# Optimization experiments

Measured on AMD Instinct MI355X. Metric: run time of the kernel, lower is better.

## Reference

```python
import jax, jax.numpy as jnp
import numpy as np

B, S, D = 4, 2048, 512   # batch, seq_len, head_size (== d_model)
H = 8                    # num_heads
DH = D // H              # depth per head = 64


def setup_inputs() -> dict:
    key = jax.random.key(0)
    ks = jax.random.split(key, 11)
    sc = 1.0 / np.sqrt(D)
    inp = {
        "q": jax.random.normal(ks[0], (B, S, D), jnp.float32),
        "k": jax.random.normal(ks[1], (B, S, D), jnp.float32),
        "v": jax.random.normal(ks[2], (B, S, D), jnp.float32),
        # causal mask: 1.0 where attention is disallowed (j > i)
        "mask": jnp.triu(jnp.ones((S, S), jnp.float32), k=1)[None, None, :, :],
        "wq": jax.random.normal(ks[3], (D, D), jnp.float32) * sc,
        "bq": jnp.zeros((D,), jnp.float32),
        "wk": jax.random.normal(ks[4], (D, D), jnp.float32) * sc,
        "bk": jnp.zeros((D,), jnp.float32),
        "wv": jax.random.normal(ks[5], (D, D), jnp.float32) * sc,
        "bv": jnp.zeros((D,), jnp.float32),
        "wo": jax.random.normal(ks[6], (D, D), jnp.float32) * sc,
        "bo": jnp.zeros((D,), jnp.float32),
    }
    return inp


def _split_heads(x):
    # [B,S,D] -> [B,H,S,DH]
    return x.reshape(B, S, H, DH).transpose(0, 2, 1, 3)


def reference(q, k, v, mask, wq, bq, wk, bk, wv, bv, wo, bo):
    query = _split_heads(q @ wq + bq)
    key_h = _split_heads(k @ wk + bk)
    value = _split_heads(v @ wv + bv)

    scale = 1.0 / jnp.sqrt(jnp.asarray(DH, jnp.float32))
    scores = jnp.einsum("bhqd,bhkd->bhqk", query, key_h) * scale
    scores = scores + mask * -1e9
    attn = jax.nn.softmax(scores, axis=-1)  # [B,H,S,S]

    ctx = jnp.einsum("bhqk,bhkd->bhqd", attn, value)
    ctx = ctx.transpose(0, 2, 1, 3).reshape(B, S, D)  # concat heads
    out = ctx @ wo + bo
    return out, attn
```

## Files before the change

kernel.cpp:

```cpp
#include <hip/hip_runtime.h>

#define Bq 4
#define Sq 2048
#define Dq 512
#define Hq 8
#define DHq 64

typedef __attribute__((ext_vector_type(8))) short bf16x8;
typedef __attribute__((ext_vector_type(4))) float floatx4;

__device__ __forceinline__ unsigned short f2bf(float f) {
    union { float f; unsigned u; } v; v.f = f;
    return (unsigned short)((v.u + 0x7fffu + ((v.u >> 16) & 1u)) >> 16);
}

template <bool OUT_BF16>
__global__ __launch_bounds__(256) void gemm_bias(
    const float* A0, const float* A1, const float* A2,
    const float* W0, const float* W1, const float* W2,
    const float* b0, const float* b1, const float* b2,
    unsigned short* O0, unsigned short* O1, unsigned short* O2,
    float* F0, float* F1, float* F2) {
  const int bz = blockIdx.z;
  const float* A = (bz == 0) ? A0 : (bz == 1) ? A1 : A2;
  const float* W = (bz == 0) ? W0 : (bz == 1) ? W1 : W2;
  const float* bias = (bz == 0) ? b0 : (bz == 1) ? b1 : b2;
  unsigned short* O = (bz == 0) ? O0 : (bz == 1) ? O1 : O2;
  float* F = (bz == 0) ? F0 : (bz == 1) ? F1 : F2;

  const int bm = blockIdx.x;
  const int bn = blockIdx.y;
  const int tid = threadIdx.x;
  const int lane = tid & 63;
  const int w = tid >> 6;
  const int wm = w >> 1;
  const int wn = w & 1;
  const int lg = lane >> 4;
  const int lc = lane & 15;

  __shared__ unsigned short As[4096];
  __shared__ unsigned short Bs[4096];

  floatx4 acc[4][4];
#pragma unroll
  for (int mt = 0; mt < 4; ++mt)
#pragma unroll
    for (int nt = 0; nt < 4; ++nt) acc[mt][nt] = (floatx4){0.f, 0.f, 0.f, 0.f};

  for (int kt = 0; kt < 16; ++kt) {
    __syncthreads();
#pragma unroll
    for (int it = 0; it < 4; ++it) {
      int idx = tid + it * 256;
      int m = idx >> 3;
      int k0 = (idx & 7) << 2;
      const float4 va =
          *(const float4*)(A + (size_t)(bm * 128 + m) * 512 + kt * 32 + k0);
      union { unsigned short u[4]; uint2 v; } pk;
      pk.u[0] = f2bf(va.x); pk.u[1] = f2bf(va.y);
      pk.u[2] = f2bf(va.z); pk.u[3] = f2bf(va.w);
      *(uint2*)&As[((((k0 >> 3) * 128 + m)) << 3) + (k0 & 7)] = pk.v;
    }
#pragma unroll
    for (int it = 0; it < 4; ++it) {
      int e = tid + it * 256;
      int n = e & 127;
      int k0 = (e >> 7) << 2;
      union { unsigned short u[4]; uint2 v; } pk;
#pragma unroll
      for (int u = 0; u < 4; ++u)
        pk.u[u] = f2bf(W[(size_t)(kt * 32 + k0 + u) * 512 + bn * 128 + n]);
      *(uint2*)&Bs[((((k0 >> 3) * 128 + n)) << 3) + (k0 & 7)] = pk.v;
    }
    __syncthreads();

    bf16x8 af[4], bfr[4];
#pragma unroll
    for (int mt = 0; mt < 4; ++mt)
      af[mt] = *(const bf16x8*)&As[(lg * 128 + wm * 64 + mt * 16 + lc) << 3];
#pragma unroll
    for (int nt = 0; nt < 4; ++nt)
      bfr[nt] = *(const bf16x8*)&Bs[(lg * 128 + wn * 64 + nt * 16 + lc) << 3];
#pragma unroll
    for (int mt = 0; mt < 4; ++mt)
#pragma unroll
      for (int nt = 0; nt < 4; ++nt)
        acc[mt][nt] = __builtin_amdgcn_mfma_f32_16x16x32_bf16(
            af[mt], bfr[nt], acc[mt][nt], 0, 0, 0);
  }

#pragma unroll
  for (int mt = 0; mt < 4; ++mt) {
#pragma unroll
    for (int nt = 0; nt < 4; ++nt) {
      int col = bn * 128 + wn * 64 + nt * 16 + lc;
      float bv = bias[col];
#pragma unroll
      for (int r = 0; r < 4; ++r) {
        int row = bm * 128 + wm * 64 + mt * 16 + lg * 4 + r;
        float val = acc[mt][nt][r] + bv;
        if (OUT_BF16)
          O[(size_t)row * 512 + col] = f2bf(val);
        else
          F[(size_t)row * 512 + col] = val;
      }
    }
  }
}

__global__ __launch_bounds__(256) void attn_kernel(
    const unsigned short* Qb, const unsigned short* Kb,
    const unsigned short* Vb, float* attn, float* ctx) {
  const int qt = blockIdx.x;
  const int h = blockIdx.y;
  const int b = blockIdx.z;
  const int qb = qt * 64;
  const int tid = threadIdx.x;
  const int lane = tid & 63;
  const int w = tid >> 6;
  const int lg = lane >> 4;
  const int lc = lane & 15;

  __shared__ unsigned short Qs[4096], Ks[4096], Vs[4096], Ps[4096];

#pragma unroll
  for (int it = 0; it < 2; ++it) {
    int cc = tid + it * 256;
    int koct = cc & 7, m = cc >> 3;
    *(uint4*)&Qs[((koct << 6) + m) << 3] =
        *(const uint4*)&Qb[(size_t)(b * Sq + qb + m) * Dq + h * DHq +
                           (koct << 3)];
  }
  __syncthreads();

  bf16x8 aQ[2];
#pragma unroll
  for (int ks = 0; ks < 2; ++ks)
    aQ[ks] = *(const bf16x8*)&Qs[(((ks * 4 + lg) << 6) + (w * 16 + lc)) << 3];

  float mrun[4] = {-1e30f, -1e30f, -1e30f, -1e30f};
  float lrun[4] = {0.f, 0.f, 0.f, 0.f};
  const int qi_base = qb + w * 16 + lg * 4;

  for (int jt = 0; jt <= qt; ++jt) {
    __syncthreads();
#pragma unroll
    for (int it = 0; it < 2; ++it) {
      int cc = tid + it * 256;
      int koct = cc & 7, m = cc >> 3;
      *(uint4*)&Ks[((koct << 6) + m) << 3] =
          *(const uint4*)&Kb[(size_t)(b * Sq + jt * 64 + m) * Dq + h * DHq +
                             (koct << 3)];
    }
    __syncthreads();

    floatx4 s[4];
#pragma unroll
    for (int nt = 0; nt < 4; ++nt) s[nt] = (floatx4){0.f, 0.f, 0.f, 0.f};
#pragma unroll
    for (int ks = 0; ks < 2; ++ks)
#pragma unroll
      for (int nt = 0; nt < 4; ++nt) {
        bf16x8 bk =
            *(const bf16x8*)&Ks[(((ks * 4 + lg) << 6) + nt * 16 + lc) << 3];
        s[nt] = __builtin_amdgcn_mfma_f32_16x16x32_bf16(aQ[ks], bk, s[nt], 0,
                                                        0, 0);
      }

#pragma unroll
    for (int r = 0; r < 4; ++r) {
      int qi = qi_base + r;
      float sv[4];
      float mx = -1e30f;
#pragma unroll
      for (int nt = 0; nt < 4; ++nt) {
        float x = s[nt][r] * 0.125f;
        int kj = jt * 64 + nt * 16 + lc;
        if (kj > qi) x = -1e30f;
        sv[nt] = x;
        mx = fmaxf(mx, x);
      }
#pragma unroll
      for (int off = 1; off < 16; off <<= 1)
        mx = fmaxf(mx, __shfl_xor(mx, off, 16));
      float mnew = fmaxf(mrun[r], mx);
      float sum = 0.f;
#pragma unroll
      for (int nt = 0; nt < 4; ++nt) sum += __expf(sv[nt] - mnew);
#pragma unroll
      for (int off = 1; off < 16; off <<= 1) sum += __shfl_xor(sum, off, 16);
      lrun[r] = lrun[r] * __expf(mrun[r] - mnew) + sum;
      mrun[r] = mnew;
    }
  }

  float rinv[4];
#pragma unroll
  for (int r = 0; r < 4; ++r) rinv[r] = 1.0f / lrun[r];

  floatx4 ctxa[4];
#pragma unroll
  for (int nt = 0; nt < 4; ++nt) ctxa[nt] = (floatx4){0.f, 0.f, 0.f, 0.f};

  float* attn_base = attn + (size_t)(b * Hq + h) * Sq * Sq;

  for (int jt = 0; jt <= qt; ++jt) {
    __syncthreads();
#pragma unroll
    for (int it = 0; it < 2; ++it) {
      int cc = tid + it * 256;
      int koct = cc & 7, m = cc >> 3;
      *(uint4*)&Ks[((koct << 6) + m) << 3] =
          *(const uint4*)&Kb[(size_t)(b * Sq + jt * 64 + m) * Dq + h * DHq +
                             (koct << 3)];
    }
#pragma unroll
    for (int it = 0; it < 2; ++it) {
      int cc = tid + it * 256;
      int dim = cc & 63, koct = cc >> 6;
      union { unsigned short u[8]; uint4 v; } pk;
#pragma unroll
      for (int u = 0; u < 8; ++u)
        pk.u[u] = Vb[(size_t)(b * Sq + jt * 64 + koct * 8 + u) * Dq + h * DHq +
                     dim];
      *(uint4*)&Vs[((koct << 6) + dim) << 3] = pk.v;
    }
    __syncthreads();

    floatx4 s[4];
#pragma unroll
    for (int nt = 0; nt < 4; ++nt) s[nt] = (floatx4){0.f, 0.f, 0.f, 0.f};
#pragma unroll
    for (int ks = 0; ks < 2; ++ks)
#pragma unroll
      for (int nt = 0; nt < 4; ++nt) {
        bf16x8 bk =
            *(const bf16x8*)&Ks[(((ks * 4 + lg) << 6) + nt * 16 + lc) << 3];
        s[nt] = __builtin_amdgcn_mfma_f32_16x16x32_bf16(aQ[ks], bk, s[nt], 0,
                                                        0, 0);
      }

#pragma unroll
    for (int r = 0; r < 4; ++r) {
      int qi = qi_base + r;
      float* arow = attn_base + (size_t)qi * Sq + jt * 64;
#pragma unroll
      for (int nt = 0; nt < 4; ++nt) {
        int kj = jt * 64 + nt * 16 + lc;
        float x = s[nt][r] * 0.125f;
        float p = (kj > qi) ? 0.f : __expf(x - mrun[r]) * rinv[r];
        arow[nt * 16 + lc] = p;
        int kk = nt * 16 + lc;
        Ps[w * 1024 + (((kk >> 3) * 16 + lg * 4 + r) << 3) + (kk & 7)] =
            f2bf(p);
      }
    }

#pragma unroll
    for (int ks = 0; ks < 2; ++ks) {
      bf16x8 ap =
          *(const bf16x8*)&Ps[w * 1024 + (((ks * 4 + lg) * 16 + lc) << 3)];
#pragma unroll
      for (int nt = 0; nt < 4; ++nt) {
        bf16x8 bv =
            *(const bf16x8*)&Vs[(((ks * 4 + lg) << 6) + nt * 16 + lc) << 3];
        ctxa[nt] = __builtin_amdgcn_mfma_f32_16x16x32_bf16(ap, bv, ctxa[nt],
                                                           0, 0, 0);
      }
    }
  }

#pragma unroll
  for (int nt = 0; nt < 4; ++nt)
#pragma unroll
    for (int r = 0; r < 4; ++r) {
      int qi = qi_base + r;
      ctx[(size_t)(b * Sq + qi) * Dq + h * DHq + nt * 16 + lc] = ctxa[nt][r];
    }

  int zc0 = qb + 64;
  int ncol4 = (Sq - zc0) >> 2;
  if (ncol4 > 0) {
    for (int rr = 0; rr < 64; ++rr) {
      float4* rowp = (float4*)(attn_base + (size_t)(qb + rr) * Sq + zc0);
      for (int c4 = tid; c4 < ncol4; c4 += 256)
        rowp[c4] = make_float4(0.f, 0.f, 0.f, 0.f);
    }
  }
}

extern "C" void kernel_launch(void* const* d_in, const int* in_sizes, int n_in,
                              void* d_out, int out_size, void* d_ws,
                              size_t ws_size, hipStream_t stream) {
  const float* q = (const float*)d_in[0];
  const float* k = (const float*)d_in[1];
  const float* v = (const float*)d_in[2];
  const float* wq = (const float*)d_in[4];
  const float* bq = (const float*)d_in[5];
  const float* wk = (const float*)d_in[6];
  const float* bk = (const float*)d_in[7];
  const float* wv = (const float*)d_in[8];
  const float* bv = (const float*)d_in[9];
  const float* wo = (const float*)d_in[10];
  const float* bo = (const float*)d_in[11];

  float* out = (float*)d_out;
  float* attn = out + (size_t)Bq * Sq * Dq;

  unsigned short* Qb = (unsigned short*)d_ws;
  unsigned short* Kb = Qb + (size_t)Bq * Sq * Dq;
  unsigned short* Vb = Kb + (size_t)Bq * Sq * Dq;
  float* ctx = (float*)(Vb + (size_t)Bq * Sq * Dq);

  dim3 blk(256);
  dim3 g1(64, 4, 3);
  gemm_bias<true><<<g1, blk, 0, stream>>>(q, k, v, wq, wk, wv, bq, bk, bv, Qb,
                                          Kb, Vb, nullptr, nullptr, nullptr);

  dim3 g2(Sq / 64, Hq, Bq);
  attn_kernel<<<g2, blk, 0, stream>>>(Qb, Kb, Vb, attn, ctx);

  dim3 g3(64, 4, 1);
  gemm_bias<false><<<g3, blk, 0, stream>>>(
      ctx, nullptr, nullptr, wo, nullptr, nullptr, bo, nullptr, nullptr,
      nullptr, nullptr, nullptr, out, nullptr, nullptr);
}
```

Baseline: 797.7 us.

## Pre-transpose V, stage attn rows in LDS for float4 stores, skip mask off-diagonal

Adds a separate kernel that transposes V per head into a [B,H,DH,S] buffer, so the attention kernel loads V tiles with 16-byte vector reads instead of scalar strided gathers. The probability tile is staged in a padded fp32 LDS buffer and written to the attention output as coalesced float4 row segments instead of scattered scalar stores. Causal-mask checks are skipped for tiles strictly below the diagonal. This costs an extra kernel launch, extra workspace, and about 17 KB more LDS per block, which may lower occupancy.

```diff
diff --git a/kernel.cpp b/kernel.cpp
--- a/kernel.cpp
+++ b/kernel.cpp
@@ -108,9 +108,39 @@
   }
 }
 
+__global__ __launch_bounds__(256) void vtrans_kernel(
+    const unsigned short* Vb, unsigned short* Vt) {
+  const int st = blockIdx.x;
+  const int h = blockIdx.y;
+  const int b = blockIdx.z;
+  const int tid = threadIdx.x;
+
+  __shared__ unsigned short T[64 * 72];
+
+#pragma unroll
+  for (int it = 0; it < 2; ++it) {
+    int idx = tid + it * 256;
+    int srow = idx >> 3, koct = idx & 7;
+    *(uint4*)&T[srow * 72 + koct * 8] =
+        *(const uint4*)&Vb[(size_t)(b * Sq + st * 64 + srow) * Dq + h * DHq +
+                           koct * 8];
+  }
+  __syncthreads();
+#pragma unroll
+  for (int it = 0; it < 2; ++it) {
+    int idx = tid + it * 256;
+    int drow = idx >> 3, soct = idx & 7;
+    union { unsigned short u[8]; uint4 v; } pk;
+#pragma unroll
+    for (int j = 0; j < 8; ++j) pk.u[j] = T[(soct * 8 + j) * 72 + drow];
+    *(uint4*)&Vt[(size_t)((b * Hq + h) * DHq + drow) * Sq + st * 64 +
+                 soct * 8] = pk.v;
+  }
+}
+
 __global__ __launch_bounds__(256) void attn_kernel(
     const unsigned short* Qb, const unsigned short* Kb,
-    const unsigned short* Vb, float* attn, float* ctx) {
+    const unsigned short* Vt, float* attn, float* ctx) {
   const int qt = blockIdx.x;
   const int h = blockIdx.y;
   const int b = blockIdx.z;
@@ -122,6 +152,7 @@
   const int lc = lane & 15;
 
   __shared__ unsigned short Qs[4096], Ks[4096], Vs[4096], Ps[4096];
+  __shared__ float Pf[4 * 1088];
 
 #pragma unroll
   for (int it = 0; it < 2; ++it) {
@@ -167,30 +198,54 @@
                                                         0, 0);
       }
 
-#pragma unroll
-    for (int r = 0; r < 4; ++r) {
-      int qi = qi_base + r;
-      float sv[4];
-      float mx = -1e30f;
-#pragma unroll
-      for (int nt = 0; nt < 4; ++nt) {
-        float x = s[nt][r] * 0.125f;
-        int kj = jt * 64 + nt * 16 + lc;
-        if (kj > qi) x = -1e30f;
-        sv[nt] = x;
-        mx = fmaxf(mx, x);
-      }
-#pragma unroll
-      for (int off = 1; off < 16; off <<= 1)
-        mx = fmaxf(mx, __shfl_xor(mx, off, 16));
-      float mnew = fmaxf(mrun[r], mx);
-      float sum = 0.f;
-#pragma unroll
-      for (int nt = 0; nt < 4; ++nt) sum += __expf(sv[nt] - mnew);
-#pragma unroll
-      for (int off = 1; off < 16; off <<= 1) sum += __shfl_xor(sum, off, 16);
-      lrun[r] = lrun[r] * __expf(mrun[r] - mnew) + sum;
-      mrun[r] = mnew;
+    if (jt < qt) {
+#pragma unroll
+      for (int r = 0; r < 4; ++r) {
+        float sv[4];
+        float mx = -1e30f;
+#pragma unroll
+        for (int nt = 0; nt < 4; ++nt) {
+          sv[nt] = s[nt][r] * 0.125f;
+          mx = fmaxf(mx, sv[nt]);
+        }
+#pragma unroll
+        for (int off = 1; off < 16; off <<= 1)
+          mx = fmaxf(mx, __shfl_xor(mx, off, 16));
+        float mnew = fmaxf(mrun[r], mx);
+        float sum = 0.f;
+#pragma unroll
+        for (int nt = 0; nt < 4; ++nt) sum += __expf(sv[nt] - mnew);
+#pragma unroll
+        for (int off = 1; off < 16; off <<= 1) sum += __shfl_xor(sum, off, 16);
+        lrun[r] = lrun[r] * __expf(mrun[r] - mnew) + sum;
+        mrun[r] = mnew;
+      }
+    } else {
+#pragma unroll
+      for (int r = 0; r < 4; ++r) {
+        int qi = qi_base + r;
+        float sv[4];
+        float mx = -1e30f;
+#pragma unroll
+        for (int nt = 0; nt < 4; ++nt) {
+          float x = s[nt][r] * 0.125f;
+          int kj = jt * 64 + nt * 16 + lc;
+          if (kj > qi) x = -1e30f;
+          sv[nt] = x;
+          mx = fmaxf(mx, x);
+        }
+#pragma unroll
+        for (int off = 1; off < 16; off <<= 1)
+          mx = fmaxf(mx, __shfl_xor(mx, off, 16));
+        float mnew = fmaxf(mrun[r], mx);
+        float sum = 0.f;
+#pragma unroll
+        for (int nt = 0; nt < 4; ++nt) sum += __expf(sv[nt] - mnew);
+#pragma unroll
+        for (int off = 1; off < 16; off <<= 1) sum += __shfl_xor(sum, off, 16);
+        lrun[r] = lrun[r] * __expf(mrun[r] - mnew) + sum;
+        mrun[r] = mnew;
+      }
     }
   }
 
@@ -203,6 +258,8 @@
   for (int nt = 0; nt < 4; ++nt) ctxa[nt] = (floatx4){0.f, 0.f, 0.f, 0.f};
 
   float* attn_base = attn + (size_t)(b * Hq + h) * Sq * Sq;
+  const int srow = lane >> 2;
+  const int sc0 = lane & 3;
 
   for (int jt = 0; jt <= qt; ++jt) {
     __syncthreads();
@@ -217,13 +274,10 @@
 #pragma unroll
     for (int it = 0; it < 2; ++it) {
       int cc = tid + it * 256;
-      int dim = cc & 63, koct = cc >> 6;
-      union { unsigned short u[8]; uint4 v; } pk;
-#pragma unroll
-      for (int u = 0; u < 8; ++u)
-        pk.u[u] = Vb[(size_t)(b * Sq + jt * 64 + koct * 8 + u) * Dq + h * DHq +
-                     dim];
-      *(uint4*)&Vs[((koct << 6) + dim) << 3] = pk.v;
+      int koct = cc & 7, dim = cc >> 3;
+      *(uint4*)&Vs[((koct << 6) + dim) << 3] =
+          *(const uint4*)&Vt[(size_t)((b * Hq + h) * DHq + dim) * Sq +
+                             jt * 64 + (koct << 3)];
     }
     __syncthreads();
 
@@ -240,19 +294,42 @@
                                                         0, 0);
       }
 
-#pragma unroll
-    for (int r = 0; r < 4; ++r) {
-      int qi = qi_base + r;
-      float* arow = attn_base + (size_t)qi * Sq + jt * 64;
-#pragma unroll
-      for (int nt = 0; nt < 4; ++nt) {
-        int kj = jt * 64 + nt * 16 + lc;
-        float x = s[nt][r] * 0.125f;
-        float p = (kj > qi) ? 0.f : __expf(x - mrun[r]) * rinv[r];
-        arow[nt * 16 + lc] = p;
-        int kk = nt * 16 + lc;
-        Ps[w * 1024 + (((kk >> 3) * 16 + lg * 4 + r) << 3) + (kk & 7)] =
-            f2bf(p);
+    if (jt < qt) {
+#pragma unroll
+      for (int r = 0; r < 4; ++r) {
+#pragma unroll
+        for (int nt = 0; nt < 4; ++nt) {
+          float p = __expf(s[nt][r] * 0.125f - mrun[r]) * rinv[r];
+          int kk = nt * 16 + lc;
+          Pf[w * 1088 + (lg * 4 + r) * 68 + kk] = p;
+          Ps[w * 1024 + (((kk >> 3) * 16 + lg * 4 + r) << 3) + (kk & 7)] =
+              f2bf(p);
+        }
+      }
+    } else {
+#pragma unroll
+      for (int r = 0; r < 4; ++r) {
+        int qi = qi_base + r;
+#pragma unroll
+        for (int nt = 0; nt < 4; ++nt) {
+          int kj = jt * 64 + nt * 16 + lc;
+          float p = (kj > qi) ? 0.f
+                              : __expf(s[nt][r] * 0.125f - mrun[r]) * rinv[r];
+          int kk = nt * 16 + lc;
+          Pf[w * 1088 + (lg * 4 + r) * 68 + kk] = p;
+          Ps[w * 1024 + (((kk >> 3) * 16 + lg * 4 + r) << 3) + (kk & 7)] =
+              f2bf(p);
+        }
+      }
+    }
+
+    {
+      float* arow = attn_base + (size_t)(qb + w * 16 + srow) * Sq + jt * 64;
+#pragma unroll
+      for (int it = 0; it < 4; ++it) {
+        int c = sc0 + it * 4;
+        float4 pv = *(float4*)&Pf[w * 1088 + srow * 68 + c * 4];
+        *(float4*)&arow[c * 4] = pv;
       }
     }
 
@@ -307,18 +384,23 @@
   float* out = (float*)d_out;
   float* attn = out + (size_t)Bq * Sq * Dq;
 
+  const size_t NE = (size_t)Bq * Sq * Dq;
   unsigned short* Qb = (unsigned short*)d_ws;
-  unsigned short* Kb = Qb + (size_t)Bq * Sq * Dq;
-  unsigned short* Vb = Kb + (size_t)Bq * Sq * Dq;
-  float* ctx = (float*)(Vb + (size_t)Bq * Sq * Dq);
+  unsigned short* Kb = Qb + NE;
+  unsigned short* Vb = Kb + NE;
+  unsigned short* Vt = Vb + NE;
+  float* ctx = (float*)(Vt + NE);
 
   dim3 blk(256);
   dim3 g1(64, 4, 3);
   gemm_bias<true><<<g1, blk, 0, stream>>>(q, k, v, wq, wk, wv, bq, bk, bv, Qb,
                                           Kb, Vb, nullptr, nullptr, nullptr);
 
+  dim3 gt(Sq / 64, Hq, Bq);
+  vtrans_kernel<<<gt, blk, 0, stream>>>(Vb, Vt);
+
   dim3 g2(Sq / 64, Hq, Bq);
-  attn_kernel<<<g2, blk, 0, stream>>>(Qb, Kb, Vb, attn, ctx);
+  attn_kernel<<<g2, blk, 0, stream>>>(Qb, Kb, Vt, attn, ctx);
 
   dim3 g3(64, 4, 1);
   gemm_bias<false><<<g3, blk, 0, stream>>>(
```

Measured after the change: 814.8 us. 2.2% more time.
